# Kernel optimization log

Hardware: AMD Instinct MI355X
Metric: run time of the kernel (lower is better)

The kernel has to match this reference:

```python
import jax, jax.numpy as jnp
import numpy as np

PH, PW = 7, 7            # output_size
SCALE = 0.25             # spatial_scale
SR = 2                   # sampling_ratio (fixed, jit-static)
ALIGNED = True


def setup_inputs() -> dict:
    key = jax.random.key(0)
    k1, k2, k3, k4, k5 = jax.random.split(key, 5)
    B, C, H, W = 4, 256, 200, 200
    N = 512
    img = H / SCALE  # 800.0 image size
    x = jax.random.normal(k1, (B, C, H, W), dtype=jnp.float32)
    bidx = jax.random.randint(k2, (N,), 0, B).astype(jnp.float32)
    cxy = jax.random.uniform(k3, (N, 2), minval=0.0, maxval=img)
    wh = jax.random.uniform(k4, (N, 2), minval=32.0, maxval=256.0)
    x1y1 = jnp.clip(cxy - wh / 2, 0.0, img - 1.0)
    x2y2 = jnp.clip(cxy + wh / 2, 0.0, img - 1.0)
    rois = jnp.concatenate([bidx[:, None], x1y1[:, 0:1], x1y1[:, 1:2],
                            x2y2[:, 0:1], x2y2[:, 1:2]], axis=1).astype(jnp.float32)
    return {"input": x, "rois": rois}


def _axis_samples(start, bin_size, P, size):
    """Sample coords along one axis. start/bin_size: [N]. Returns per-sample
    low/high integer indices, interp weights, and validity mask, all [N, P*SR]."""
    ib = jnp.arange(P, dtype=jnp.float32)           # bin index
    isr = jnp.arange(SR, dtype=jnp.float32)         # sample within bin
    # coord[n, p, s] = start + p*bin + (s+0.5)*bin/SR
    coord = (start[:, None, None]
             + ib[None, :, None] * bin_size[:, None, None]
             + (isr[None, None, :] + 0.5) * bin_size[:, None, None] / SR)
    coord = coord.reshape(coord.shape[0], P * SR)
    valid = (coord >= -1.0) & (coord <= size)
    c = jnp.maximum(coord, 0.0)
    lo_raw = jnp.floor(c).astype(jnp.int32)
    at_edge = lo_raw >= size - 1
    lo = jnp.where(at_edge, size - 1, lo_raw)
    hi = jnp.where(at_edge, size - 1, lo_raw + 1)
    cv = jnp.where(at_edge, jnp.float32(size - 1), c)
    frac = cv - lo.astype(jnp.float32)              # weight toward hi
    return lo, hi, frac, valid


def reference(input, rois):
    B, C, H, W = input.shape
    N = rois.shape[0]
    b = rois[:, 0].astype(jnp.int32)
    off = 0.5 if ALIGNED else 0.0
    sx = rois[:, 1] * SCALE - off
    sy = rois[:, 2] * SCALE - off
    ex = rois[:, 3] * SCALE - off
    ey = rois[:, 4] * SCALE - off
    rw, rh = ex - sx, ey - sy
    if not ALIGNED:
        rw = jnp.maximum(rw, 1.0)
        rh = jnp.maximum(rh, 1.0)
    bin_w, bin_h = rw / PW, rh / PH

    yl, yh, fy, vy = _axis_samples(sy, bin_h, PH, H)   # [N, Sy]
    xl, xh, fx, vx = _axis_samples(sx, bin_w, PW, W)   # [N, Sx]

    featT = jnp.transpose(input, (0, 2, 3, 1))         # [B,H,W,C]

    def gather(yi, xi):  # -> [N, Sy, Sx, C]
        return featT[b[:, None, None], yi[:, :, None], xi[:, None, :]]

    hy, ly = (1.0 - fy), fy
    hx, lx = (1.0 - fx), fx
    w_ll = (hy[:, :, None] * hx[:, None, :])[..., None]
    w_lh = (hy[:, :, None] * lx[:, None, :])[..., None]
    w_hl = (ly[:, :, None] * hx[:, None, :])[..., None]
    w_hh = (ly[:, :, None] * lx[:, None, :])[..., None]

    val = (w_ll * gather(yl, xl) + w_lh * gather(yl, xh)
           + w_hl * gather(yh, xl) + w_hh * gather(yh, xh))
    mask = (vy[:, :, None] & vx[:, None, :])[..., None]
    val = jnp.where(mask, val, 0.0)                    # [N, Sy, Sx, C]

    # average pool the SRxSR samples per output bin
    val = val.reshape(N, PH, SR, PW, SR, C).mean(axis=(2, 4))  # [N,PH,PW,C]
    return jnp.transpose(val, (0, 3, 1, 2))            # [N,C,PH,PW]
```

## Files before the change

### kernel.cpp

```cpp
#include <hip/hip_runtime.h>


#define R_PH 7
#define R_PW 7
#define R_SR 2
#define R_SCALE 0.25f
#define R_C 256
#define R_H 200
#define R_W 200
#define R_HW (R_H * R_W)
#define STRIP 50
#define NSTRIP 4
#define STAGE_ROWS 56

__device__ __forceinline__ void axis_sample(float start, float bin, int p, int s, int size,
                                            int& lo, int& hi, float& wlo, float& whi) {
    float coord = (start + (float)p * bin) + ((float)s + 0.5f) * bin * (1.0f / R_SR);
    bool valid = (coord >= -1.0f) && (coord <= (float)size);
    float c = fmaxf(coord, 0.0f);
    int lo_raw = (int)floorf(c);
    bool at_edge = lo_raw >= size - 1;
    lo = at_edge ? size - 1 : lo_raw;
    hi = at_edge ? size - 1 : lo_raw + 1;
    float cv = at_edge ? (float)(size - 1) : c;
    float frac = cv - (float)lo;
    whi = valid ? frac : 0.0f;
    wlo = valid ? (1.0f - frac) : 0.0f;
}

__global__ void __launch_bounds__(512)
build_lists(const float* __restrict__ rois, int N, int* __restrict__ ws) {
    __shared__ int lcnt[NSTRIP * 4];
    int t = threadIdx.x;
    if (t < 16) lcnt[t] = 0;
    __syncthreads();
    int* lists = ws + 16;
    for (int n = t; n < N; n += 512) {
        const float* r = rois + (size_t)n * 5;
        int b = (int)r[0];
        float sy = r[2] * R_SCALE - 0.5f;
        float ey = r[4] * R_SCALE - 0.5f;
        float binh = (ey - sy) * (1.0f / R_PH);
        for (int ph = 0; ph < R_PH; ++ph) {
            int lo, hi; float wl, wh;
            axis_sample(sy, binh, ph, 0, R_H, lo, hi, wl, wh);
            int bs = b * NSTRIP + lo / STRIP;
            int pos = atomicAdd(&lcnt[bs], 1);
            lists[bs * (N * R_PH) + pos] = (n << 3) | ph;
        }
    }
    __syncthreads();
    if (t < 16) ws[t] = lcnt[t];
}

__global__ void __launch_bounds__(512)
roi_strip(const float* __restrict__ input,
          const float* __restrict__ rois,
          const int* __restrict__ ws, int N,
          float* __restrict__ out) {
    __shared__ float pl[STAGE_ROWS * R_W];
    int c = blockIdx.x;
    int b = blockIdx.y;
    int s = blockIdx.z;
    int r0 = s * STRIP;
    int nrows = min(STAGE_ROWS, R_H - r0);

    const float4* src = (const float4*)(input + (size_t)(b * R_C + c) * R_HW + r0 * R_W);
    float4* dstv = (float4*)pl;
    int nf4 = nrows * (R_W / 4);
    for (int i = threadIdx.x; i < nf4; i += 512) dstv[i] = src[i];

    int m = ws[b * NSTRIP + s];
    const int* list = ws + 16 + (b * NSTRIP + s) * (N * R_PH);
    __syncthreads();

    int total = m * R_PW;
    for (int i = threadIdx.x; i < total; i += 512) {
        int e  = i / R_PW;
        int pw = i - e * R_PW;
        int code = list[e];
        int n  = code >> 3;
        int ph = code & 7;
        const float* r = rois + (size_t)n * 5;
        float sx = r[1] * R_SCALE - 0.5f;
        float sy = r[2] * R_SCALE - 0.5f;
        float ex = r[3] * R_SCALE - 0.5f;
        float ey = r[4] * R_SCALE - 0.5f;
        float binw = (ex - sx) * (1.0f / R_PW);
        float binh = (ey - sy) * (1.0f / R_PH);

        int   ylo[R_SR], yhi[R_SR], xlo[R_SR], xhi[R_SR];
        float wyl[R_SR], wyh[R_SR], wxl[R_SR], wxh[R_SR];
#pragma unroll
        for (int q = 0; q < R_SR; ++q) {
            axis_sample(sy, binh, ph, q, R_H, ylo[q], yhi[q], wyl[q], wyh[q]);
            axis_sample(sx, binw, pw, q, R_W, xlo[q], xhi[q], wxl[q], wxh[q]);
        }

        float acc = 0.0f;
#pragma unroll
        for (int ys = 0; ys < R_SR; ++ys) {
            const float* rlo = pl + (ylo[ys] - r0) * R_W;
            const float* rhi = pl + (yhi[ys] - r0) * R_W;
#pragma unroll
            for (int xs = 0; xs < R_SR; ++xs) {
                acc += wyl[ys] * (wxl[xs] * rlo[xlo[xs]] + wxh[xs] * rlo[xhi[xs]])
                     + wyh[ys] * (wxl[xs] * rhi[xlo[xs]] + wxh[xs] * rhi[xhi[xs]]);
            }
        }
        out[(size_t)(n * R_C + c) * 49 + ph * R_PW + pw] = acc * 0.25f;
    }
}

__global__ void __launch_bounds__(256)
roi_align_fwd(const float* __restrict__ input,
              const float* __restrict__ rois,
              float* __restrict__ out, int total) {
    int idx = blockIdx.x * blockDim.x + threadIdx.x;
    if (idx >= total) return;
    int pw = idx % R_PW;
    int ph = (idx / R_PW) % R_PH;
    int c  = (idx / (R_PW * R_PH)) % R_C;
    int n  = idx / (R_PW * R_PH * R_C);
    const float* r = rois + (size_t)n * 5;
    int   b  = (int)r[0];
    float sx = r[1] * R_SCALE - 0.5f;
    float sy = r[2] * R_SCALE - 0.5f;
    float ex = r[3] * R_SCALE - 0.5f;
    float ey = r[4] * R_SCALE - 0.5f;
    float bin_w = (ex - sx) * (1.0f / R_PW);
    float bin_h = (ey - sy) * (1.0f / R_PH);
    const float* plane = input + (size_t)(b * R_C + c) * R_HW;
    int   ylo[R_SR], yhi[R_SR], xlo[R_SR], xhi[R_SR];
    float wylo[R_SR], wyhi[R_SR], wxlo[R_SR], wxhi[R_SR];
#pragma unroll
    for (int s = 0; s < R_SR; ++s) {
        axis_sample(sy, bin_h, ph, s, R_H, ylo[s], yhi[s], wylo[s], wyhi[s]);
        axis_sample(sx, bin_w, pw, s, R_W, xlo[s], xhi[s], wxlo[s], wxhi[s]);
    }
    float acc = 0.0f;
#pragma unroll
    for (int ys = 0; ys < R_SR; ++ys) {
        const float* row_lo = plane + ylo[ys] * R_W;
        const float* row_hi = plane + yhi[ys] * R_W;
#pragma unroll
        for (int xs = 0; xs < R_SR; ++xs) {
            acc += wylo[ys] * (wxlo[xs] * row_lo[xlo[xs]] + wxhi[xs] * row_lo[xhi[xs]])
                 + wyhi[ys] * (wxlo[xs] * row_hi[xlo[xs]] + wxhi[xs] * row_hi[xhi[xs]]);
        }
    }
    out[idx] = acc * (1.0f / (R_SR * R_SR));
}

extern "C" void kernel_launch(void* const* d_in, const int* in_sizes, int n_in,
                              void* d_out, int out_size, void* d_ws, size_t ws_size,
                              hipStream_t stream) {
    const float* input = (const float*)d_in[0];
    const float* rois  = (const float*)d_in[1];
    float* out = (float*)d_out;
    int N = in_sizes[1] / 5;

    size_t ws_needed = (size_t)(16 + 16 * N * R_PH) * sizeof(int);
    if (ws_size >= ws_needed) {
        int* ws = (int*)d_ws;
        build_lists<<<1, 512, 0, stream>>>(rois, N, ws);
        dim3 grid(R_C, 4, NSTRIP);
        roi_strip<<<grid, 512, 0, stream>>>(input, rois, ws, N, out);
    } else {
        int total = out_size;
        roi_align_fwd<<<(total + 255) / 256, 256, 0, stream>>>(input, rois, out, total);
    }
}
```

Measured before the change: 260.1 us.

## Halve ROI strip height and precompute per-ROI sample index/weight tables

New measurement: 275.2 us. +5.8%, slower.

```diff
diff --git a/kernel.cpp b/kernel.cpp
--- a/kernel.cpp
+++ b/kernel.cpp
@@ -9,9 +9,10 @@
 #define R_H 200
 #define R_W 200
 #define R_HW (R_H * R_W)
-#define STRIP 50
-#define NSTRIP 4
-#define STAGE_ROWS 56
+#define STRIP 25
+#define NSTRIP 8
+#define NLISTS 32
+#define STAGE_ROWS 31
 
 __device__ __forceinline__ void axis_sample(float start, float bin, int p, int s, int size,
                                             int& lo, int& hi, float& wlo, float& whi) {
@@ -30,32 +31,46 @@
 
 __global__ void __launch_bounds__(512)
 build_lists(const float* __restrict__ rois, int N, int* __restrict__ ws) {
-    __shared__ int lcnt[NSTRIP * 4];
+    __shared__ int lcnt[NLISTS];
     int t = threadIdx.x;
-    if (t < 16) lcnt[t] = 0;
+    if (t < NLISTS) lcnt[t] = 0;
     __syncthreads();
-    int* lists = ws + 16;
+    int*    lists = ws + NLISTS;
+    int4*   yrows = (int4*)(lists + NLISTS * N * R_PH);
+    float4* yw    = (float4*)(yrows + N * R_PH);
+    int4*   xcols = (int4*)(yw + N * R_PH);
+    float4* xw    = (float4*)(xcols + N * R_PH);
+
     for (int n = t; n < N; n += 512) {
         const float* r = rois + (size_t)n * 5;
         int b = (int)r[0];
+        float sx = r[1] * R_SCALE - 0.5f;
         float sy = r[2] * R_SCALE - 0.5f;
+        float ex = r[3] * R_SCALE - 0.5f;
         float ey = r[4] * R_SCALE - 0.5f;
+        float binw = (ex - sx) * (1.0f / R_PW);
         float binh = (ey - sy) * (1.0f / R_PH);
-        for (int ph = 0; ph < R_PH; ++ph) {
-            int lo, hi; float wl, wh;
-            axis_sample(sy, binh, ph, 0, R_H, lo, hi, wl, wh);
-            int bs = b * NSTRIP + lo / STRIP;
+        for (int p = 0; p < R_PH; ++p) {
+            int lo0, hi0, lo1, hi1; float wl0, wh0, wl1, wh1;
+            axis_sample(sy, binh, p, 0, R_H, lo0, hi0, wl0, wh0);
+            axis_sample(sy, binh, p, 1, R_H, lo1, hi1, wl1, wh1);
+            yrows[n * R_PH + p] = make_int4(lo0 * R_W, hi0 * R_W, lo1 * R_W, hi1 * R_W);
+            yw[n * R_PH + p]    = make_float4(wl0 * 0.25f, wh0 * 0.25f, wl1 * 0.25f, wh1 * 0.25f);
+            int bs = b * NSTRIP + lo0 / STRIP;
             int pos = atomicAdd(&lcnt[bs], 1);
-            lists[bs * (N * R_PH) + pos] = (n << 3) | ph;
+            lists[bs * (N * R_PH) + pos] = (n << 3) | p;
+            axis_sample(sx, binw, p, 0, R_W, lo0, hi0, wl0, wh0);
+            axis_sample(sx, binw, p, 1, R_W, lo1, hi1, wl1, wh1);
+            xcols[n * R_PH + p] = make_int4(lo0, hi0, lo1, hi1);
+            xw[n * R_PH + p]    = make_float4(wl0, wh0, wl1, wh1);
         }
     }
     __syncthreads();
-    if (t < 16) ws[t] = lcnt[t];
+    if (t < NLISTS) ws[t] = lcnt[t];
 }
 
 __global__ void __launch_bounds__(512)
 roi_strip(const float* __restrict__ input,
-          const float* __restrict__ rois,
           const int* __restrict__ ws, int N,
           float* __restrict__ out) {
     __shared__ float pl[STAGE_ROWS * R_W];
@@ -71,9 +86,15 @@
     for (int i = threadIdx.x; i < nf4; i += 512) dstv[i] = src[i];
 
     int m = ws[b * NSTRIP + s];
-    const int* list = ws + 16 + (b * NSTRIP + s) * (N * R_PH);
+    const int*    lists = ws + NLISTS;
+    const int*    list  = lists + (b * NSTRIP + s) * (N * R_PH);
+    const int4*   yrows = (const int4*)(lists + NLISTS * N * R_PH);
+    const float4* yw    = (const float4*)(yrows + N * R_PH);
+    const int4*   xcols = (const int4*)(yw + N * R_PH);
+    const float4* xw    = (const float4*)(xcols + N * R_PH);
     __syncthreads();
 
+    int r0b = r0 * R_W;
     int total = m * R_PW;
     for (int i = threadIdx.x; i < total; i += 512) {
         int e  = i / R_PW;
@@ -81,34 +102,21 @@
         int code = list[e];
         int n  = code >> 3;
         int ph = code & 7;
-        const float* r = rois + (size_t)n * 5;
-        float sx = r[1] * R_SCALE - 0.5f;
-        float sy = r[2] * R_SCALE - 0.5f;
-        float ex = r[3] * R_SCALE - 0.5f;
-        float ey = r[4] * R_SCALE - 0.5f;
-        float binw = (ex - sx) * (1.0f / R_PW);
-        float binh = (ey - sy) * (1.0f / R_PH);
+        int4   yr  = yrows[n * R_PH + ph];
+        float4 ywt = yw[n * R_PH + ph];
+        int4   xc  = xcols[n * R_PH + pw];
+        float4 xwt = xw[n * R_PH + pw];
 
-        int   ylo[R_SR], yhi[R_SR], xlo[R_SR], xhi[R_SR];
-        float wyl[R_SR], wyh[R_SR], wxl[R_SR], wxh[R_SR];
-#pragma unroll
-        for (int q = 0; q < R_SR; ++q) {
-            axis_sample(sy, binh, ph, q, R_H, ylo[q], yhi[q], wyl[q], wyh[q]);
-            axis_sample(sx, binw, pw, q, R_W, xlo[q], xhi[q], wxl[q], wxh[q]);
-        }
-
-        float acc = 0.0f;
-#pragma unroll
-        for (int ys = 0; ys < R_SR; ++ys) {
-            const float* rlo = pl + (ylo[ys] - r0) * R_W;
-            const float* rhi = pl + (yhi[ys] - r0) * R_W;
-#pragma unroll
-            for (int xs = 0; xs < R_SR; ++xs) {
-                acc += wyl[ys] * (wxl[xs] * rlo[xlo[xs]] + wxh[xs] * rlo[xhi[xs]])
-                     + wyh[ys] * (wxl[xs] * rhi[xlo[xs]] + wxh[xs] * rhi[xhi[xs]]);
-            }
-        }
-        out[(size_t)(n * R_C + c) * 49 + ph * R_PW + pw] = acc * 0.25f;
+        const float* p0 = pl + (yr.x - r0b);
+        const float* p1 = pl + (yr.y - r0b);
+        const float* p2 = pl + (yr.z - r0b);
+        const float* p3 = pl + (yr.w - r0b);
+        float s0 = xwt.x * p0[xc.x] + xwt.y * p0[xc.y] + xwt.z * p0[xc.z] + xwt.w * p0[xc.w];
+        float s1 = xwt.x * p1[xc.x] + xwt.y * p1[xc.y] + xwt.z * p1[xc.z] + xwt.w * p1[xc.w];
+        float s2 = xwt.x * p2[xc.x] + xwt.y * p2[xc.y] + xwt.z * p2[xc.z] + xwt.w * p2[xc.w];
+        float s3 = xwt.x * p3[xc.x] + xwt.y * p3[xc.y] + xwt.z * p3[xc.z] + xwt.w * p3[xc.w];
+        out[(size_t)(n * R_C + c) * 49 + ph * R_PW + pw] =
+            ywt.x * s0 + ywt.y * s1 + ywt.z * s2 + ywt.w * s3;
     }
 }
 
@@ -160,12 +168,12 @@
     float* out = (float*)d_out;
     int N = in_sizes[1] / 5;
 
-    size_t ws_needed = (size_t)(16 + 16 * N * R_PH) * sizeof(int);
+    size_t ws_needed = (size_t)(NLISTS + NLISTS * N * R_PH + 16 * N * R_PH) * sizeof(int);
     if (ws_size >= ws_needed) {
         int* ws = (int*)d_ws;
         build_lists<<<1, 512, 0, stream>>>(rois, N, ws);
         dim3 grid(R_C, 4, NSTRIP);
-        roi_strip<<<grid, 512, 0, stream>>>(input, rois, ws, N, out);
+        roi_strip<<<grid, 512, 0, stream>>>(input, ws, N, out);
     } else {
         int total = out_size;
         roi_align_fwd<<<(total + 255) / 256, 256, 0, stream>>>(input, rois, out, total);
```
